# Performance work log

Hardware: AMD Instinct MI355X
Metric: run time of the kernel (lower is better)

The kernel has to match this reference:

```python
import jax, jax.numpy as jnp
import numpy as np

N_TILES, NX = 6, 96
IN_C, HID_C = 128, 256
BATCH = 4


def _build_neighbors(n_tiles=N_TILES, nx=NX):
    # 4-connectivity on each tile with periodic wrap (fixed cubed-sphere-style
    # grid graph; preserves the gather/mean access pattern of build_dgl_graph).
    i, j = np.meshgrid(np.arange(nx), np.arange(nx), indexing='ij')
    idx = lambda ii, jj: (ii % nx) * nx + (jj % nx)
    per_tile = np.stack([idx(i - 1, j), idx(i + 1, j), idx(i, j - 1), idx(i, j + 1)],
                        axis=-1).reshape(nx * nx, 4)
    offsets = (np.arange(n_tiles) * nx * nx)[:, None, None]
    return (per_tile[None] + offsets).reshape(-1, 4).astype(np.int32)


def setup_inputs() -> dict:
    key = jax.random.key(0)
    ks = jax.random.split(key, 6)
    s = lambda fan_in: 1.0 / np.sqrt(fan_in)
    return {
        'x': jax.random.normal(ks[0], (BATCH, N_TILES, NX, NX, IN_C), jnp.float32),
        'neighbors': jnp.asarray(_build_neighbors()),
        'W_self1': jax.random.normal(ks[1], (IN_C, HID_C), jnp.float32) * s(IN_C),
        'W_neigh1': jax.random.normal(ks[2], (IN_C, HID_C), jnp.float32) * s(IN_C),
        'b1': jnp.zeros((HID_C,), jnp.float32),
        'W_self2': jax.random.normal(ks[3], (HID_C, HID_C), jnp.float32) * s(HID_C),
        'W_neigh2': jax.random.normal(ks[4], (HID_C, HID_C), jnp.float32) * s(HID_C),
        'b2': jnp.zeros((HID_C,), jnp.float32),
    }


def _sage_conv(h, neighbors, W_self, W_neigh, b):
    # h: [B, N, C]; neighbors: [N, 4] -> mean-aggregated SAGEConv
    h_neigh = jnp.mean(h[:, neighbors], axis=2)  # [B, N, 4, C] -> [B, N, C]
    return jnp.einsum('bnc,cd->bnd', h, W_self) + \
           jnp.einsum('bnc,cd->bnd', h_neigh, W_neigh) + b


def reference(x, neighbors, W_self1, W_neigh1, b1, W_self2, W_neigh2, b2):
    B, T, X, Y, C = x.shape
    h = x.reshape(B, T * X * Y, C)                      # flatten sphere -> nodes
    h = jax.nn.relu(_sage_conv(h, neighbors, W_self1, W_neigh1, b1))
    h = jax.nn.relu(_sage_conv(h, neighbors, W_self2, W_neigh2, b2))
    return h.reshape(B, T, X, Y, -1)
```

## Files before the change

### kernel.cpp

```cpp
#include <hip/hip_runtime.h>
#include <stdint.h>

typedef __attribute__((ext_vector_type(8))) short short8;
typedef __attribute__((ext_vector_type(4))) float f32x4;

#define NNODES 55296
#define DOUT 256

#define WAIT_VM(N) asm volatile("s_waitcnt vmcnt(" #N ")" ::: "memory")
#define SOFT_FENCE asm volatile("" ::: "memory")

__device__ __forceinline__ float bf2f(unsigned short h) {
    union { unsigned u; float f; } x; x.u = ((unsigned)h) << 16; return x.f;
}
__device__ __forceinline__ unsigned short f2bf(float f) {
    union { float f; unsigned u; } x; x.f = f;
    return (unsigned short)((x.u + 0x7fffu + ((x.u >> 16) & 1u)) >> 16);
}

__device__ __forceinline__ void storev(float* p, float v) { *p = v; }
__device__ __forceinline__ void storev(unsigned short* p, float v) { *p = f2bf(v); }

__device__ __forceinline__ void dma16(const void* g, void* l) {
    __builtin_amdgcn_global_load_lds(
        reinterpret_cast<const unsigned int __attribute__((address_space(1)))*>((uintptr_t)g),
        reinterpret_cast<unsigned int __attribute__((address_space(3)))*>((uintptr_t)l),
        16, 0, 0);
}

__device__ __forceinline__ short8 frag_self(const float* p) {
    float4 a = *(const float4*)p, b = *(const float4*)(p + 4);
    union { short8 s; unsigned short u[8]; } r;
    r.u[0] = f2bf(a.x); r.u[1] = f2bf(a.y); r.u[2] = f2bf(a.z); r.u[3] = f2bf(a.w);
    r.u[4] = f2bf(b.x); r.u[5] = f2bf(b.y); r.u[6] = f2bf(b.z); r.u[7] = f2bf(b.w);
    return r.s;
}
__device__ __forceinline__ short8 frag_self(const unsigned short* p) {
    return *(const short8*)p;
}
__device__ __forceinline__ void acc8(const float* p, float* o) {
    float4 a = *(const float4*)p, b = *(const float4*)(p + 4);
    o[0] += a.x; o[1] += a.y; o[2] += a.z; o[3] += a.w;
    o[4] += b.x; o[5] += b.y; o[6] += b.z; o[7] += b.w;
}
__device__ __forceinline__ void acc8(const unsigned short* p, float* o) {
    uint4 v = *(const uint4*)p;
    const unsigned short* u = (const unsigned short*)&v;
#pragma unroll
    for (int i = 0; i < 8; ++i) o[i] += bf2f(u[i]);
}
template <typename TIN>
__device__ __forceinline__ short8 frag_mean4(const TIN* p0, const TIN* p1,
                                             const TIN* p2, const TIN* p3) {
    float s[8] = {0.f, 0.f, 0.f, 0.f, 0.f, 0.f, 0.f, 0.f};
    acc8(p0, s); acc8(p1, s); acc8(p2, s); acc8(p3, s);
    union { short8 s8; unsigned short u[8]; } r;
#pragma unroll
    for (int i = 0; i < 8; ++i) r.u[i] = f2bf(s[i] * 0.25f);
    return r.s8;
}

__global__ void build_wt(const float* __restrict__ Ws,
                         const float* __restrict__ Wn,
                         unsigned short* __restrict__ Wt, int C) {
    int K2 = 2 * C;
    int idx = blockIdx.x * 256 + threadIdx.x;
    if (idx >= 256 * K2) return;
    int d = idx / K2;
    int k = idx - d * K2;
    float v = (k < C) ? Ws[(size_t)k * DOUT + d] : Wn[(size_t)(k - C) * DOUT + d];
    Wt[idx] = f2bf(v);
}

__global__ __launch_bounds__(256) void mean_xb(const float* __restrict__ x,
                                               const int* __restrict__ nbr,
                                               unsigned short* __restrict__ xm) {
    const int idx = blockIdx.x * 256 + threadIdx.x;
    const int node = idx >> 4;
    const int ch = (idx & 15) * 8;
    const int b = node / NNODES;
    const int n = node - b * NNODES;
    const size_t bbase = (size_t)b * NNODES;
    const int4 nb = *(const int4*)(nbr + (size_t)n * 4);
    const float* ps = x + (size_t)node * 128 + ch;
    union { uint4 v; unsigned short u[8]; } rs, rm;
    float4 a0 = *(const float4*)ps, a1 = *(const float4*)(ps + 4);
    rs.u[0] = f2bf(a0.x); rs.u[1] = f2bf(a0.y); rs.u[2] = f2bf(a0.z); rs.u[3] = f2bf(a0.w);
    rs.u[4] = f2bf(a1.x); rs.u[5] = f2bf(a1.y); rs.u[6] = f2bf(a1.z); rs.u[7] = f2bf(a1.w);
    float s[8] = {0.f, 0.f, 0.f, 0.f, 0.f, 0.f, 0.f, 0.f};
    acc8(x + (bbase + nb.x) * 128 + ch, s);
    acc8(x + (bbase + nb.y) * 128 + ch, s);
    acc8(x + (bbase + nb.z) * 128 + ch, s);
    acc8(x + (bbase + nb.w) * 128 + ch, s);
#pragma unroll
    for (int i = 0; i < 8; ++i) rm.u[i] = f2bf(s[i] * 0.25f);
    *(uint4*)(xm + (size_t)node * 256 + ch) = rs.v;
    *(uint4*)(xm + (size_t)node * 256 + 128 + ch) = rm.v;
}

template <int C, typename TIN>
__global__ __launch_bounds__(256) void mean_pass(const TIN* __restrict__ hin,
                                                 const int* __restrict__ nbr,
                                                 unsigned short* __restrict__ hm) {
    constexpr int CPL = C / 8;
    const int idx = blockIdx.x * 256 + threadIdx.x;
    const int node = idx / CPL;
    const int ch = (idx - node * CPL) * 8;
    const int b = node / NNODES;
    const int n = node - b * NNODES;
    const size_t bbase = (size_t)b * NNODES;
    const int4 nb = *(const int4*)(nbr + (size_t)n * 4);
    float s[8] = {0.f, 0.f, 0.f, 0.f, 0.f, 0.f, 0.f, 0.f};
    acc8(hin + (bbase + nb.x) * (size_t)C + ch, s);
    acc8(hin + (bbase + nb.y) * (size_t)C + ch, s);
    acc8(hin + (bbase + nb.z) * (size_t)C + ch, s);
    acc8(hin + (bbase + nb.w) * (size_t)C + ch, s);
    union { uint4 v; unsigned short u[8]; } r;
#pragma unroll
    for (int i = 0; i < 8; ++i) r.u[i] = f2bf(s[i] * 0.25f);
    *(uint4*)(hm + (size_t)node * C + ch) = r.v;
}

__global__ __launch_bounds__(512) void sage_v8_l1(
    const unsigned short* __restrict__ xm,
    const unsigned short* __restrict__ Wt,
    const float* __restrict__ bias,
    unsigned short* __restrict__ out) {
    extern __shared__ char lds[];
    const int tid = threadIdx.x;
    const int rowbase = blockIdx.x * 256;
    const int l = tid & 63, w = tid >> 6;
    const int lr = l & 15, lg = l >> 4;
    const int rowg = w >> 1;
    const int colb = (w & 1) * 128;
    const char* wsrc = (const char*)Wt;
    const char* xb = (const char*)xm;

    auto stageW = [&](int s) {
#pragma unroll
        for (int i = 0; i < 8; ++i) {
            int o = (tid + i * 512) * 16;
            int col = o >> 8, kb = o & 255;
            uint4 v = *(const uint4*)(wsrc + (size_t)col * 512 + s * 256 + kb);
            *(uint4*)(lds + (o ^ ((col & 7) << 4))) = v;
        }
    };
    auto issueA = [&](int p) {
        const int kb = p * 64;
        char* ldst = lds + 65536 + (p & 3) * 16384 + w * 1024;
#pragma unroll
        for (int i = 0; i < 2; ++i) {
            int c = tid + i * 512;
            int row = c >> 2, slot = c & 3;
            const char* src = xb + (size_t)(rowbase + row) * 512 + kb +
                              ((slot ^ (row & 3)) << 4);
            dma16(src, ldst + i * 8192);
        }
    };

    issueA(0); issueA(1); issueA(2);
    stageW(0);
    __syncthreads();

    f32x4 acc[4][8];
#pragma unroll
    for (int m = 0; m < 4; ++m)
#pragma unroll
        for (int j = 0; j < 8; ++j) acc[m][j] = (f32x4){0.f, 0.f, 0.f, 0.f};

    int arow0[4];
#pragma unroll
    for (int m = 0; m < 4; ++m) arow0[m] = rowg * 64 + m * 16 + lr;

#pragma unroll
    for (int kk = 0; kk < 8; ++kk) {
        if (kk <= 5) { WAIT_VM(4); }
        else if (kk == 6) { WAIT_VM(2); }
        else { WAIT_VM(0); }
        __builtin_amdgcn_s_barrier();
        SOFT_FENCE;
        if (kk == 4) {
            stageW(1);
            __syncthreads();
        }
        if (kk + 3 < 8) issueA(kk + 3);

        const int bufo = 65536 + (kk & 3) * 16384;
        short8 af[4];
#pragma unroll
        for (int m = 0; m < 4; ++m) {
            const int ar = arow0[m];
            af[m] = *(const short8*)(lds + bufo + ar * 64 + ((lg ^ (ar & 3)) << 4));
        }
#pragma unroll
        for (int j = 0; j < 8; ++j) {
            const int col = colb + j * 16 + lr;
            const short8 wf = *(const short8*)(
                lds + ((col * 256 + (kk & 3) * 64 + lg * 16) ^ ((col & 7) << 4)));
#pragma unroll
            for (int m = 0; m < 4; ++m)
                acc[m][j] = __builtin_amdgcn_mfma_f32_16x16x32_bf16(wf, af[m], acc[m][j], 0, 0, 0);
        }
        SOFT_FENCE;
    }

#pragma unroll
    for (int m = 0; m < 4; ++m) {
        const int row = rowbase + rowg * 64 + m * 16 + lr;
#pragma unroll
        for (int j = 0; j < 8; ++j) {
            const int c0 = colb + j * 16 + lg * 4;
            const float4 bv = *(const float4*)(bias + c0);
            union { unsigned short u[4]; uint2 v; } pk;
            pk.u[0] = f2bf(fmaxf(acc[m][j][0] + bv.x, 0.f));
            pk.u[1] = f2bf(fmaxf(acc[m][j][1] + bv.y, 0.f));
            pk.u[2] = f2bf(fmaxf(acc[m][j][2] + bv.z, 0.f));
            pk.u[3] = f2bf(fmaxf(acc[m][j][3] + bv.w, 0.f));
            *(uint2*)(out + (size_t)row * 256 + c0) = pk.v;
        }
    }
}

__global__ __launch_bounds__(512) void sage_v8_l2(
    const unsigned short* __restrict__ h1p,
    const unsigned short* __restrict__ hmp,
    const unsigned short* __restrict__ Wt,
    const float* __restrict__ bias,
    float* __restrict__ out) {
    extern __shared__ char lds[];
    const int tid = threadIdx.x;
    const int bid = blockIdx.x;
    const int yg = bid & 1;
    const int rb = bid >> 1;
    const int gcol0 = yg * 128;
    const int rowbase = rb * 256;

    const int l = tid & 63;
    const int w = tid >> 6;
    const int lr = l & 15, lg = l >> 4;
    const int rowg = w >> 1;
    const int colb = (w & 1) * 64;

    const char* wsrc = (const char*)Wt + (size_t)gcol0 * 1024;

    auto stageW = [&](int s) {
#pragma unroll
        for (int i = 0; i < 8; ++i) {
            int o = (tid + i * 512) * 16;
            int col = o >> 9, kb = o & 511;
            uint4 v = *(const uint4*)(wsrc + (size_t)col * 1024 + s * 512 + kb);
            *(uint4*)(lds + (o ^ ((col & 7) << 4))) = v;
        }
    };

    auto issueA = [&](int p) {
        const char* base = (p < 8) ? (const char*)h1p : (const char*)hmp;
        const int kb = (p & 7) * 64;
        char* ldst = lds + 65536 + (p & 3) * 16384 + w * 1024;
#pragma unroll
        for (int i = 0; i < 2; ++i) {
            int c = tid + i * 512;
            int row = c >> 2, slot = c & 3;
            const char* src = base + (size_t)(rowbase + row) * 512 + kb +
                              ((slot ^ (row & 3)) << 4);
            dma16(src, ldst + i * 8192);
        }
    };

    issueA(0); issueA(1); issueA(2);
    stageW(0);
    __syncthreads();

    f32x4 acc[4][4];
#pragma unroll
    for (int m = 0; m < 4; ++m)
#pragma unroll
        for (int j = 0; j < 4; ++j) acc[m][j] = (f32x4){0.f, 0.f, 0.f, 0.f};

    int arow0[4];
#pragma unroll
    for (int m = 0; m < 4; ++m) arow0[m] = rowg * 64 + m * 16 + lr;

#pragma unroll
    for (int kk = 0; kk < 16; ++kk) {
        if (kk <= 13) { WAIT_VM(4); }
        else if (kk == 14) { WAIT_VM(2); }
        else { WAIT_VM(0); }
        __builtin_amdgcn_s_barrier();
        SOFT_FENCE;
        if (kk == 8) {
            stageW(1);
            __syncthreads();
        }
        if (kk + 3 < 16) issueA(kk + 3);

        const int bufo = 65536 + (kk & 3) * 16384;
        short8 af[4], wf[4];
#pragma unroll
        for (int m = 0; m < 4; ++m) {
            const int ar = arow0[m];
            af[m] = *(const short8*)(lds + bufo + ar * 64 + ((lg ^ (ar & 3)) << 4));
        }
#pragma unroll
        for (int j = 0; j < 4; ++j) {
            const int col = colb + j * 16 + lr;
            wf[j] = *(const short8*)(
                lds + (((col << 9) + ((kk & 7) << 6) + (lg << 4)) ^ ((lr & 7) << 4)));
        }
#pragma unroll
        for (int j = 0; j < 4; ++j)
#pragma unroll
            for (int m = 0; m < 4; ++m)
                acc[m][j] = __builtin_amdgcn_mfma_f32_16x16x32_bf16(wf[j], af[m], acc[m][j], 0, 0, 0);
        SOFT_FENCE;
    }

#pragma unroll
    for (int m = 0; m < 4; ++m) {
        const int row = rowbase + rowg * 64 + m * 16 + lr;
#pragma unroll
        for (int j = 0; j < 4; ++j) {
            const int gcol = gcol0 + colb + j * 16 + lg * 4;
            const float4 bv = *(const float4*)(bias + gcol);
            float4 o;
            o.x = fmaxf(acc[m][j][0] + bv.x, 0.f);
            o.y = fmaxf(acc[m][j][1] + bv.y, 0.f);
            o.z = fmaxf(acc[m][j][2] + bv.z, 0.f);
            o.w = fmaxf(acc[m][j][3] + bv.w, 0.f);
            *(float4*)(out + (size_t)row * 256 + gcol) = o;
        }
    }
}

template <int C, typename TIN, typename TOUT>
__global__ __launch_bounds__(512, 2) void sage_v3(
    const TIN* __restrict__ hin, const int* __restrict__ nbr,
    const unsigned short* __restrict__ Wt, const float* __restrict__ bias,
    TOUT* __restrict__ out) {
    constexpr int K2 = 2 * C;
    constexpr int ROWB = K2 * 2;
    constexpr int LCOLS = 131072 / ROWB;
    constexpr int CG = LCOLS / 128;
    constexpr int RG = 8 / CG;
    extern __shared__ char Bs[];

    const int tid = threadIdx.x;
    const int gcol0 = blockIdx.y * LCOLS;
    {
        const char* src = (const char*)(Wt + (size_t)gcol0 * K2);
#pragma unroll
        for (int i = 0; i < 16; ++i) {
            int byt = (i * 512 + tid) * 16;
            uint4 v = *(const uint4*)(src + byt);
            int c = byt / ROWB;
            *(uint4*)(Bs + (byt ^ ((c & 7) << 4))) = v;
        }
    }
    __syncthreads();

    const int l = tid & 63;
    const int w = tid >> 6;
    const int rowg = w / CG;
    const int colb = (w % CG) * 128;
    const int lr = l & 15, lg = l >> 4;

    const int rowbase = blockIdx.x * (RG * 64) + rowg * 64;
    const int bb = rowbase / NNODES;
    const int n0 = rowbase - bb * NNODES;
    const size_t bbase = (size_t)bb * NNODES;

    unsigned soff[4], noff[4][4];
#pragma unroll
    for (int m = 0; m < 4; ++m) {
        int r = m * 16 + lr;
        soff[m] = (unsigned)(((rowbase + r) * (size_t)C + lg * 8) * sizeof(TIN));
        int4 nb = *(const int4*)(nbr + (size_t)(n0 + r) * 4);
        noff[m][0] = (unsigned)(((bbase + nb.x) * C + lg * 8) * sizeof(TIN));
        noff[m][1] = (unsigned)(((bbase + nb.y) * C + lg * 8) * sizeof(TIN));
        noff[m][2] = (unsigned)(((bbase + nb.z) * C + lg * 8) * sizeof(TIN));
        noff[m][3] = (unsigned)(((bbase + nb.w) * C + lg * 8) * sizeof(TIN));
    }
    const char* hb = (const char*)hin;

    f32x4 acc[4][8];
#pragma unroll
    for (int m = 0; m < 4; ++m)
#pragma unroll
        for (int j = 0; j < 8; ++j) acc[m][j] = (f32x4){0.f, 0.f, 0.f, 0.f};

#pragma unroll
    for (int kk = 0; kk < K2 / 32; ++kk) {
        const int k0 = kk * 32;
        short8 a[4];
        if (k0 < C) {
            const unsigned kb = k0 * sizeof(TIN);
#pragma unroll
            for (int m = 0; m < 4; ++m)
                a[m] = frag_self((const TIN*)(hb + soff[m] + kb));
        } else {
            const unsigned kb = (k0 - C) * sizeof(TIN);
#pragma unroll
            for (int m = 0; m < 4; ++m)
                a[m] = frag_mean4((const TIN*)(hb + noff[m][0] + kb),
                                  (const TIN*)(hb + noff[m][1] + kb),
                                  (const TIN*)(hb + noff[m][2] + kb),
                                  (const TIN*)(hb + noff[m][3] + kb));
        }
#pragma unroll
        for (int j = 0; j < 8; ++j) {
            const int c = colb + j * 16 + lr;
            const short8 bf = *(const short8*)(
                Bs + ((c * ROWB + (k0 + lg * 8) * 2) ^ ((l & 7) << 4)));
#pragma unroll
            for (int m = 0; m < 4; ++m)
                acc[m][j] = __builtin_amdgcn_mfma_f32_16x16x32_bf16(a[m], bf, acc[m][j], 0, 0, 0);
        }
    }

#pragma unroll
    for (int j = 0; j < 8; ++j) {
        const int gcol = gcol0 + colb + j * 16 + lr;
        const float bv = bias[gcol];
#pragma unroll
        for (int m = 0; m < 4; ++m) {
#pragma unroll
            for (int r = 0; r < 4; ++r) {
                const int row = rowbase + m * 16 + lg * 4 + r;
                storev(out + (size_t)row * DOUT + gcol, fmaxf(acc[m][j][r] + bv, 0.f));
            }
        }
    }
}

extern "C" void kernel_launch(void* const* d_in, const int* in_sizes, int n_in,
                              void* d_out, int out_size, void* d_ws, size_t ws_size,
                              hipStream_t stream) {
    const float* x = (const float*)d_in[0];
    const int* nbr = (const int*)d_in[1];
    const float* Ws1 = (const float*)d_in[2];
    const float* Wn1 = (const float*)d_in[3];
    const float* b1 = (const float*)d_in[4];
    const float* Ws2 = (const float*)d_in[5];
    const float* Wn2 = (const float*)d_in[6];
    const float* b2 = (const float*)d_in[7];
    float* out = (float*)d_out;

    const int B = in_sizes[0] / (NNODES * 128);
    const int M = B * NNODES;

    char* ws = (char*)d_ws;
    const size_t h1_bytes = (size_t)M * DOUT * 2;
    const size_t hm_bytes = (size_t)M * DOUT * 2;
    const size_t need = h1_bytes + hm_bytes + 131072 + 262144;

    if (ws_size >= need) {
        unsigned short* h1 = (unsigned short*)ws;
        unsigned short* xm = (unsigned short*)(ws + h1_bytes);
        unsigned short* Wt1 = (unsigned short*)(ws + h1_bytes + hm_bytes);
        unsigned short* Wt2 = Wt1 + 256 * 256;

        build_wt<<<256, 256, 0, stream>>>(Ws1, Wn1, Wt1, 128);
        build_wt<<<512, 256, 0, stream>>>(Ws2, Wn2, Wt2, 256);

        hipFuncSetAttribute((const void*)sage_v8_l1,
                            hipFuncAttributeMaxDynamicSharedMemorySize, 131072);
        hipFuncSetAttribute((const void*)sage_v8_l2,
                            hipFuncAttributeMaxDynamicSharedMemorySize, 131072);

        mean_xb<<<M / 16, 256, 0, stream>>>(x, nbr, xm);
        sage_v8_l1<<<M / 256, 512, 131072, stream>>>(xm, Wt1, b1, h1);
        mean_pass<256, unsigned short><<<M * 32 / 256, 256, 0, stream>>>(h1, nbr, xm);
        sage_v8_l2<<<(M / 256) * 2, 512, 131072, stream>>>(h1, xm, Wt2, b2, out);
    } else {
        unsigned short* h1 = (unsigned short*)ws;
        unsigned short* Wt1 = (unsigned short*)(ws + h1_bytes);
        unsigned short* Wt2 = Wt1 + 256 * 256;

        build_wt<<<256, 256, 0, stream>>>(Ws1, Wn1, Wt1, 128);
        build_wt<<<512, 256, 0, stream>>>(Ws2, Wn2, Wt2, 256);

        hipFuncSetAttribute((const void*)sage_v3<128, float, unsigned short>,
                            hipFuncAttributeMaxDynamicSharedMemorySize, 131072);
        hipFuncSetAttribute((const void*)sage_v3<256, unsigned short, float>,
                            hipFuncAttributeMaxDynamicSharedMemorySize, 131072);

        sage_v3<128, float, unsigned short>
            <<<dim3(M / 256, 1), 512, 131072, stream>>>(x, nbr, Wt1, b1, h1);
        sage_v3<256, unsigned short, float>
            <<<dim3(M / 512, 2), 512, 131072, stream>>>(h1, nbr, Wt2, b2, out);
    }
}
```

Measured before the change: 345.7 us.

## Shrink GEMM LDS footprint with chunked weight DMA and triple-buffered A

Both GEMM kernels now stage weights in 256-byte K chunks through async global-to-LDS DMA instead of register round-trips. The A operand moves from four ring buffers to three. Total LDS drops from 128 KiB to 80 KiB per block, which is meant to let more blocks share a CU. Layer 1 is also split into two column halves per row tile, doubling the grid and halving accumulators. The cost is extra barriers for each weight restage and a shallower prefetch depth (two tiles ahead instead of three).

```diff
diff --git a/kernel.cpp b/kernel.cpp
--- a/kernel.cpp
+++ b/kernel.cpp
@@ -8,6 +8,7 @@
 #define DOUT 256
 
 #define WAIT_VM(N) asm volatile("s_waitcnt vmcnt(" #N ")" ::: "memory")
+#define WAIT_LGKM0 asm volatile("s_waitcnt lgkmcnt(0)" ::: "memory")
 #define SOFT_FENCE asm volatile("" ::: "memory")
 
 __device__ __forceinline__ float bf2f(unsigned short h) {
@@ -121,52 +122,56 @@
     *(uint4*)(hm + (size_t)node * C + ch) = r.v;
 }
 
-__global__ __launch_bounds__(512) void sage_v8_l1(
+
+__global__ __launch_bounds__(512, 4) void sage_v9_l1(
     const unsigned short* __restrict__ xm,
     const unsigned short* __restrict__ Wt,
     const float* __restrict__ bias,
     unsigned short* __restrict__ out) {
     extern __shared__ char lds[];
     const int tid = threadIdx.x;
-    const int rowbase = blockIdx.x * 256;
+    const int bid = blockIdx.x;
+    const int yg = bid & 1;
+    const int rb = bid >> 1;
+    const int gcol0 = yg * 128;
+    const int rowbase = rb * 256;
+
     const int l = tid & 63, w = tid >> 6;
     const int lr = l & 15, lg = l >> 4;
     const int rowg = w >> 1;
-    const int colb = (w & 1) * 128;
-    const char* wsrc = (const char*)Wt;
+    const int colb = (w & 1) * 64;
+
+    const char* wsrc = (const char*)Wt + (size_t)gcol0 * 512;
     const char* xb = (const char*)xm;
 
     auto stageW = [&](int s) {
 #pragma unroll
-        for (int i = 0; i < 8; ++i) {
-            int o = (tid + i * 512) * 16;
-            int col = o >> 8, kb = o & 255;
-            uint4 v = *(const uint4*)(wsrc + (size_t)col * 512 + s * 256 + kb);
-            *(uint4*)(lds + (o ^ ((col & 7) << 4))) = v;
+        for (int i = 0; i < 4; ++i) {
+            int o = w * 4096 + i * 1024 + l * 16;
+            int col = o >> 8, kq = o & 255;
+            dma16(wsrc + (size_t)col * 512 + s * 256 + (kq ^ ((col & 7) << 4)),
+                  lds + w * 4096 + i * 1024);
         }
     };
     auto issueA = [&](int p) {
         const int kb = p * 64;
-        char* ldst = lds + 65536 + (p & 3) * 16384 + w * 1024;
+        char* ldst = lds + 32768 + (p % 3) * 16384 + w * 1024;
 #pragma unroll
         for (int i = 0; i < 2; ++i) {
             int c = tid + i * 512;
             int row = c >> 2, slot = c & 3;
-            const char* src = xb + (size_t)(rowbase + row) * 512 + kb +
-                              ((slot ^ (row & 3)) << 4);
-            dma16(src, ldst + i * 8192);
+            dma16(xb + (size_t)(rowbase + row) * 512 + kb + ((slot ^ (row & 3)) << 4),
+                  ldst + i * 8192);
         }
     };
 
-    issueA(0); issueA(1); issueA(2);
-    stageW(0);
-    __syncthreads();
-
-    f32x4 acc[4][8];
+    issueA(0); stageW(0); issueA(1);
+
+    f32x4 acc[4][4];
 #pragma unroll
     for (int m = 0; m < 4; ++m)
 #pragma unroll
-        for (int j = 0; j < 8; ++j) acc[m][j] = (f32x4){0.f, 0.f, 0.f, 0.f};
+        for (int j = 0; j < 4; ++j) acc[m][j] = (f32x4){0.f, 0.f, 0.f, 0.f};
 
     int arow0[4];
 #pragma unroll
@@ -174,33 +179,37 @@
 
 #pragma unroll
     for (int kk = 0; kk < 8; ++kk) {
-        if (kk <= 5) { WAIT_VM(4); }
-        else if (kk == 6) { WAIT_VM(2); }
-        else { WAIT_VM(0); }
+        if (kk == 7) { WAIT_VM(0); } else { WAIT_VM(2); }
         __builtin_amdgcn_s_barrier();
         SOFT_FENCE;
-        if (kk == 4) {
-            stageW(1);
-            __syncthreads();
-        }
-        if (kk + 3 < 8) issueA(kk + 3);
-
-        const int bufo = 65536 + (kk & 3) * 16384;
-        short8 af[4];
+
+        const int bufo = 32768 + (kk % 3) * 16384;
+        short8 af[4], wf[4];
 #pragma unroll
         for (int m = 0; m < 4; ++m) {
             const int ar = arow0[m];
             af[m] = *(const short8*)(lds + bufo + ar * 64 + ((lg ^ (ar & 3)) << 4));
         }
 #pragma unroll
-        for (int j = 0; j < 8; ++j) {
+        for (int j = 0; j < 4; ++j) {
             const int col = colb + j * 16 + lr;
-            const short8 wf = *(const short8*)(
-                lds + ((col * 256 + (kk & 3) * 64 + lg * 16) ^ ((col & 7) << 4)));
+            wf[j] = *(const short8*)(
+                lds + (col << 8) + ((((kk & 3) << 6) | (lg << 4)) ^ ((lr & 7) << 4)));
+        }
+
+        if (kk == 3) {
+            WAIT_LGKM0;
+            __builtin_amdgcn_sched_barrier(0);
+            __builtin_amdgcn_s_barrier();
+            stageW(1);
+        }
+        if (kk + 2 < 8) issueA(kk + 2);
+
+#pragma unroll
+        for (int j = 0; j < 4; ++j)
 #pragma unroll
             for (int m = 0; m < 4; ++m)
-                acc[m][j] = __builtin_amdgcn_mfma_f32_16x16x32_bf16(wf, af[m], acc[m][j], 0, 0, 0);
-        }
+                acc[m][j] = __builtin_amdgcn_mfma_f32_16x16x32_bf16(wf[j], af[m], acc[m][j], 0, 0, 0);
         SOFT_FENCE;
     }
 
@@ -208,8 +217,8 @@
     for (int m = 0; m < 4; ++m) {
         const int row = rowbase + rowg * 64 + m * 16 + lr;
 #pragma unroll
-        for (int j = 0; j < 8; ++j) {
-            const int c0 = colb + j * 16 + lg * 4;
+        for (int j = 0; j < 4; ++j) {
+            const int c0 = gcol0 + colb + j * 16 + lg * 4;
             const float4 bv = *(const float4*)(bias + c0);
             union { unsigned short u[4]; uint2 v; } pk;
             pk.u[0] = f2bf(fmaxf(acc[m][j][0] + bv.x, 0.f));
@@ -221,7 +230,7 @@
     }
 }
 
-__global__ __launch_bounds__(512) void sage_v8_l2(
+__global__ __launch_bounds__(512, 4) void sage_v9_l2(
     const unsigned short* __restrict__ h1p,
     const unsigned short* __restrict__ hmp,
     const unsigned short* __restrict__ Wt,
@@ -235,8 +244,7 @@
     const int gcol0 = yg * 128;
     const int rowbase = rb * 256;
 
-    const int l = tid & 63;
-    const int w = tid >> 6;
+    const int l = tid & 63, w = tid >> 6;
     const int lr = l & 15, lg = l >> 4;
     const int rowg = w >> 1;
     const int colb = (w & 1) * 64;
@@ -245,31 +253,27 @@
 
     auto stageW = [&](int s) {
 #pragma unroll
-        for (int i = 0; i < 8; ++i) {
-            int o = (tid + i * 512) * 16;
-            int col = o >> 9, kb = o & 511;
-            uint4 v = *(const uint4*)(wsrc + (size_t)col * 1024 + s * 512 + kb);
-            *(uint4*)(lds + (o ^ ((col & 7) << 4))) = v;
+        for (int i = 0; i < 4; ++i) {
+            int o = w * 4096 + i * 1024 + l * 16;
+            int col = o >> 8, kq = o & 255;
+            dma16(wsrc + (size_t)col * 1024 + s * 256 + (kq ^ ((col & 7) << 4)),
+                  lds + w * 4096 + i * 1024);
         }
     };
-
     auto issueA = [&](int p) {
         const char* base = (p < 8) ? (const char*)h1p : (const char*)hmp;
         const int kb = (p & 7) * 64;
-        char* ldst = lds + 65536 + (p & 3) * 16384 + w * 1024;
+        char* ldst = lds + 32768 + (p % 3) * 16384 + w * 1024;
 #pragma unroll
         for (int i = 0; i < 2; ++i) {
             int c = tid + i * 512;
             int row = c >> 2, slot = c & 3;
-            const char* src = base + (size_t)(rowbase + row) * 512 + kb +
-                              ((slot ^ (row & 3)) << 4);
-            dma16(src, ldst + i * 8192);
+            dma16(base + (size_t)(rowbase + row) * 512 + kb + ((slot ^ (row & 3)) << 4),
+                  ldst + i * 8192);
         }
     };
 
-    issueA(0); issueA(1); issueA(2);
-    stageW(0);
-    __syncthreads();
+    issueA(0); stageW(0); issueA(1);
 
     f32x4 acc[4][4];
 #pragma unroll
@@ -283,18 +287,11 @@
 
 #pragma unroll
     for (int kk = 0; kk < 16; ++kk) {
-        if (kk <= 13) { WAIT_VM(4); }
-        else if (kk == 14) { WAIT_VM(2); }
-        else { WAIT_VM(0); }
+        if (kk == 15) { WAIT_VM(0); } else { WAIT_VM(2); }
         __builtin_amdgcn_s_barrier();
         SOFT_FENCE;
-        if (kk == 8) {
-            stageW(1);
-            __syncthreads();
-        }
-        if (kk + 3 < 16) issueA(kk + 3);
-
-        const int bufo = 65536 + (kk & 3) * 16384;
+
+        const int bufo = 32768 + (kk % 3) * 16384;
         short8 af[4], wf[4];
 #pragma unroll
         for (int m = 0; m < 4; ++m) {
@@ -305,8 +302,17 @@
         for (int j = 0; j < 4; ++j) {
             const int col = colb + j * 16 + lr;
             wf[j] = *(const short8*)(
-                lds + (((col << 9) + ((kk & 7) << 6) + (lg << 4)) ^ ((lr & 7) << 4)));
-        }
+                lds + (col << 8) + ((((kk & 3) << 6) | (lg << 4)) ^ ((lr & 7) << 4)));
+        }
+
+        if ((kk & 3) == 3 && kk < 15) {
+            WAIT_LGKM0;
+            __builtin_amdgcn_sched_barrier(0);
+            __builtin_amdgcn_s_barrier();
+            stageW((kk >> 2) + 1);
+        }
+        if (kk + 2 < 16) issueA(kk + 2);
+
 #pragma unroll
         for (int j = 0; j < 4; ++j)
 #pragma unroll
@@ -462,15 +468,15 @@
         build_wt<<<256, 256, 0, stream>>>(Ws1, Wn1, Wt1, 128);
         build_wt<<<512, 256, 0, stream>>>(Ws2, Wn2, Wt2, 256);
 
-        hipFuncSetAttribute((const void*)sage_v8_l1,
-                            hipFuncAttributeMaxDynamicSharedMemorySize, 131072);
-        hipFuncSetAttribute((const void*)sage_v8_l2,
-                            hipFuncAttributeMaxDynamicSharedMemorySize, 131072);
+        hipFuncSetAttribute((const void*)sage_v9_l1,
+                            hipFuncAttributeMaxDynamicSharedMemorySize, 81920);
+        hipFuncSetAttribute((const void*)sage_v9_l2,
+                            hipFuncAttributeMaxDynamicSharedMemorySize, 81920);
 
         mean_xb<<<M / 16, 256, 0, stream>>>(x, nbr, xm);
-        sage_v8_l1<<<M / 256, 512, 131072, stream>>>(xm, Wt1, b1, h1);
+        sage_v9_l1<<<(M / 256) * 2, 512, 81920, stream>>>(xm, Wt1, b1, h1);
         mean_pass<256, unsigned short><<<M * 32 / 256, 256, 0, stream>>>(h1, nbr, xm);
-        sage_v8_l2<<<(M / 256) * 2, 512, 131072, stream>>>(h1, xm, Wt2, b2, out);
+        sage_v9_l2<<<(M / 256) * 2, 512, 81920, stream>>>(h1, xm, Wt2, b2, out);
     } else {
         unsigned short* h1 = (unsigned short*)ws;
         unsigned short* Wt1 = (unsigned short*)(ws + h1_bytes);
```

Result: slower. 384.0 us (+11.1%).
